# Performance work log

Hardware: AMD Instinct MI355X
Metric: run time of the kernel (lower is better)

## Reference

```python
import jax, jax.numpy as jnp
import numpy as np

N_NODES = 100000
FEAT = 64
HID = 128
N_EDGES = 1200000


def setup_inputs() -> dict:
    key = jax.random.key(0)
    ks = jax.random.split(key, 8)
    x = jax.random.normal(ks[0], (N_NODES, FEAT), dtype=jnp.float32)
    edge_index = jax.random.randint(ks[1], (2, N_EDGES), 0, N_NODES, dtype=jnp.int32)
    # SAGEConv params: lin_l (on aggregated neighbors, with bias), lin_r (on root, no bias)
    W1l = jax.random.normal(ks[2], (HID, FEAT), jnp.float32) / np.float32(np.sqrt(FEAT))
    b1l = jnp.zeros((HID,), jnp.float32)
    W1r = jax.random.normal(ks[3], (HID, FEAT), jnp.float32) / np.float32(np.sqrt(FEAT))
    W2l = jax.random.normal(ks[4], (FEAT, HID), jnp.float32) / np.float32(np.sqrt(HID))
    b2l = jnp.zeros((FEAT,), jnp.float32)
    W2r = jax.random.normal(ks[5], (FEAT, HID), jnp.float32) / np.float32(np.sqrt(HID))
    return {"x": x, "edge_index": edge_index, "W1l": W1l, "b1l": b1l,
            "W1r": W1r, "W2l": W2l, "b2l": b2l, "W2r": W2r}


def _sage_conv(x, src, dst, Wl, bl, Wr, n_nodes):
    # mean aggregation of neighbor messages x[src] at targets dst
    msg = x[src]                                                  # [E, d]
    agg = jax.ops.segment_sum(msg, dst, num_segments=n_nodes)     # [N, d]
    deg = jax.ops.segment_sum(jnp.ones((src.shape[0],), x.dtype), dst,
                              num_segments=n_nodes)               # [N]
    agg = agg / jnp.maximum(deg, 1.0)[:, None]
    # out = lin_l(agg) + lin_r(x); lin_r has no bias (PyG SAGEConv default)
    return agg @ Wl.T + bl + x @ Wr.T


def reference(x, edge_index, W1l, b1l, W1r, W2l, b2l, W2r):
    src, dst = edge_index[0], edge_index[1]
    n = x.shape[0]
    h = jax.nn.relu(_sage_conv(x, src, dst, W1l, b1l, W1r, n))
    # dropout(p=0.5) is identity in eval mode
    out = _sage_conv(h, src, dst, W2l, b2l, W2r, n)
    return out
```

## Files before the change

kernel.cpp:

```cpp
#include <hip/hip_runtime.h>
#include <hip/hip_bf16.h>

typedef __bf16 bf16;
typedef __attribute__((ext_vector_type(8))) __bf16 bf16x8;
typedef __attribute__((ext_vector_type(4))) float f32x4;

#define NBLK 256
#define CAP 3072

__device__ inline void unpack8(uint4 r, f32x4& a, f32x4& b) {
  a.x = __uint_as_float(r.x << 16);
  a.y = __uint_as_float(r.x & 0xffff0000u);
  a.z = __uint_as_float(r.y << 16);
  a.w = __uint_as_float(r.y & 0xffff0000u);
  b.x = __uint_as_float(r.z << 16);
  b.y = __uint_as_float(r.z & 0xffff0000u);
  b.z = __uint_as_float(r.w << 16);
  b.w = __uint_as_float(r.w & 0xffff0000u);
}

__device__ inline uint4 lslot(const bf16* __restrict__ tab, const int* lnbr,
                              int base, int e, int q, int fo) {
  int idx = base + q;
  uint4 r = make_uint4(0u, 0u, 0u, 0u);
  if (idx < e) {
    int j = lnbr[idx];
    r = *(const uint4*)(tab + (long)j * 64 + fo);
  }
  return r;
}

__global__ __launch_bounds__(256) void setup_k(const float* __restrict__ x,
                                               const int* __restrict__ dst,
                                               const float* __restrict__ W1l,
                                               const float* __restrict__ W1r,
                                               const float* __restrict__ W2l,
                                               const float* __restrict__ W2r,
                                               bf16* __restrict__ xb,
                                               bf16* __restrict__ B1,
                                               bf16* __restrict__ B2,
                                               int* __restrict__ hist,
                                               int E, int nb, int N, int Np) {
  __shared__ int h[1024];
  int t = threadIdx.x;
  if (blockIdx.x < NBLK) {
    for (int i = t; i < nb; i += 256) h[i] = 0;
    __syncthreads();
    int chunk = (E + NBLK - 1) / NBLK;
    int s = blockIdx.x * chunk, e = min(E, s + chunk);
    for (int i = s + t; i < e; i += 256) atomicAdd(&h[dst[i] >> 7], 1);
    __syncthreads();
    for (int i = t; i < nb; i += 256) hist[(long)i * NBLK + blockIdx.x] = h[i];
  } else if (blockIdx.x < NBLK + 128) {
    int gid = (blockIdx.x - NBLK) * 256 + t;
    if (gid < 16384) {
      int c = gid >> 7, k = gid & 127;
      float v = (k < 64) ? W1l[c * 64 + k] : W1r[c * 64 + (k - 64)];
      B1[gid] = (bf16)v;
    } else {
      int idx = gid - 16384;
      int n = idx >> 7, k = idx & 127;
      float v = (n < 64) ? W2l[n * 128 + k] : W2r[(n - 64) * 128 + k];
      B2[idx] = (bf16)v;
    }
  } else {
    int gid = (blockIdx.x - NBLK - 128) * 256 + t;
    long base = (long)gid * 4;
    if (base >= (long)Np * 64) return;
    if (base < (long)N * 64) {
      f32x4 v = *(const f32x4*)(x + base);
      bf16 o[4] = {(bf16)v.x, (bf16)v.y, (bf16)v.z, (bf16)v.w};
      *(ulong1*)(xb + base) = *(ulong1*)o;
    } else {
      bf16 o[4] = {(bf16)0.0f, (bf16)0.0f, (bf16)0.0f, (bf16)0.0f};
      *(ulong1*)(xb + base) = *(ulong1*)o;
    }
  }
}

__global__ __launch_bounds__(256) void scanA_k(int* __restrict__ hist,
                                               int* __restrict__ bsum) {
  __shared__ int sd[256];
  int t = threadIdx.x;
  int idx = blockIdx.x * 256 + t;
  int v = hist[idx];
  sd[t] = v;
  __syncthreads();
#pragma unroll
  for (int off = 1; off < 256; off <<= 1) {
    int tv = (t >= off) ? sd[t - off] : 0;
    __syncthreads();
    if (t >= off) sd[t] += tv;
    __syncthreads();
  }
  hist[idx] = sd[t] - v;
  if (t == 255) bsum[blockIdx.x] = sd[255];
}

__global__ __launch_bounds__(1024) void scanB_k(int* __restrict__ bsum, int nb) {
  __shared__ int sd[1024];
  int t = threadIdx.x;
  int v = (t < nb) ? bsum[t] : 0;
  sd[t] = v;
  __syncthreads();
#pragma unroll
  for (int off = 1; off < 1024; off <<= 1) {
    int tv = (t >= off) ? sd[t - off] : 0;
    __syncthreads();
    if (t >= off) sd[t] += tv;
    __syncthreads();
  }
  if (t < nb) bsum[t] = sd[t] - v;
}

__global__ __launch_bounds__(512) void scat_k(const int* __restrict__ src,
                                              const int* __restrict__ dst,
                                              const int* __restrict__ hist,
                                              const int* __restrict__ bsum,
                                              unsigned* __restrict__ ebuf, int E, int nb) {
  __shared__ int cur[1024];
  for (int i = threadIdx.x; i < nb; i += 512)
    cur[i] = bsum[i] + hist[(long)i * NBLK + blockIdx.x];
  __syncthreads();
  int chunk = (E + NBLK - 1) / NBLK;
  int s = blockIdx.x * chunk, e = min(E, s + chunk);
  for (int i = s + threadIdx.x; i < e; i += 512) {
    int d = dst[i];
    int pos = atomicAdd(&cur[d >> 7], 1);
    ebuf[pos] = ((unsigned)src[i] << 7) | (unsigned)(d & 127);
  }
}

__device__ inline void bucket_sort(const unsigned* __restrict__ ebuf, int s, int e,
                                   int t, int* hcnt, int* hoff, int* lnbr) {
  if (t < 128) hcnt[t] = 0;
  __syncthreads();
  for (int i = s + t; i < e; i += 512) atomicAdd(&hcnt[ebuf[i] & 127u], 1);
  __syncthreads();
  if (t < 128) hoff[t + 1] = hcnt[t];
  if (t == 0) hoff[0] = 0;
  __syncthreads();
#pragma unroll
  for (int off = 1; off < 128; off <<= 1) {
    int v = (t < 128 && t >= off) ? hoff[t + 1 - off] : 0;
    __syncthreads();
    if (t < 128 && t >= off) hoff[t + 1] += v;
    __syncthreads();
  }
  if (t < 128) hcnt[t] = hoff[t];
  __syncthreads();
  for (int i = s + t; i < e; i += 512) {
    unsigned r = ebuf[i];
    int pos = atomicAdd(&hcnt[r & 127u], 1);
    lnbr[pos] = (int)(r >> 7);
  }
  __syncthreads();
}

__global__ __launch_bounds__(512) void bagg1_k(const bf16* __restrict__ xb,
                                               const unsigned* __restrict__ ebuf,
                                               const int* __restrict__ bsum,
                                               bf16* __restrict__ A1, int nb, int E) {
  __shared__ int hcnt[128];
  __shared__ int hoff[129];
  __shared__ int lnbr[CAP];
  int b = blockIdx.x, t = threadIdx.x;
  int s = bsum[b];
  int e = (b + 1 < nb) ? bsum[b + 1] : E;
  if (e - s > CAP) e = s + CAP;
  bucket_sort(ebuf, s, e, t, hcnt, hoff, lnbr);

  int wave = t >> 6, lane = t & 63;
  int q = lane >> 3, f = lane & 7, fo = f * 8;
  int ls = hoff[wave * 16], le = hoff[wave * 16 + 1];
  uint4 c0 = lslot(xb, lnbr, ls, le, q, fo);
  uint4 c1 = lslot(xb, lnbr, ls + 8, le, q, fo);
  for (int mm = 0; mm < 16; mm++) {
    int lsN = 0, leN = 0;
    if (mm < 15) { lsN = hoff[wave * 16 + mm + 1]; leN = hoff[wave * 16 + mm + 2]; }
    uint4 n0 = lslot(xb, lnbr, lsN, leN, q, fo);
    uint4 n1 = lslot(xb, lnbr, lsN + 8, leN, q, fo);
    f32x4 sa = {0, 0, 0, 0}, sb = {0, 0, 0, 0};
    if (ls + 16 < le) {
      uint4 a0 = c0, a1 = c1;
      for (int i = ls + 16; i < le; i += 16) {
        uint4 t0 = lslot(xb, lnbr, i, le, q, fo);
        uint4 t1 = lslot(xb, lnbr, i + 8, le, q, fo);
        f32x4 a, bb;
        unpack8(a0, a, bb); sa += a; sb += bb;
        unpack8(a1, a, bb); sa += a; sb += bb;
        a0 = t0; a1 = t1;
      }
      c0 = a0; c1 = a1;
    }
    {
      f32x4 a, bb;
      unpack8(c0, a, bb); sa += a; sb += bb;
      unpack8(c1, a, bb); sa += a; sb += bb;
    }
    float v[8] = {sa.x, sa.y, sa.z, sa.w, sb.x, sb.y, sb.z, sb.w};
#pragma unroll
    for (int k = 0; k < 8; k++) {
      v[k] += __shfl_xor(v[k], 8);
      v[k] += __shfl_xor(v[k], 16);
      v[k] += __shfl_xor(v[k], 32);
    }
    long n = (long)b * 128 + wave * 16 + mm;
    float invd = 1.0f / fmaxf((float)(le - ls), 1.0f);
    if (q == 0) {
      bf16x8 o = {(bf16)(v[0] * invd), (bf16)(v[1] * invd), (bf16)(v[2] * invd),
                  (bf16)(v[3] * invd), (bf16)(v[4] * invd), (bf16)(v[5] * invd),
                  (bf16)(v[6] * invd), (bf16)(v[7] * invd)};
      *(bf16x8*)(A1 + n * 128 + fo) = o;
    } else if (q == 1) {
      uint4 rv = *(const uint4*)(xb + n * 64 + fo);
      *(uint4*)(A1 + n * 128 + 64 + fo) = rv;
    }
    c0 = n0; c1 = n1; ls = lsN; le = leN;
  }
}

__device__ inline int swzoff(int r, int x) {
  return r * 256 + (x ^ (((r & 3) << 6) ^ ((r & 7) << 4)));
}

__global__ __launch_bounds__(256) void fused_k(const bf16* __restrict__ A,
                                               const bf16* __restrict__ B1g,
                                               const bf16* __restrict__ B2g,
                                               const float* __restrict__ b1l,
                                               bf16* __restrict__ Ct,
                                               bf16* __restrict__ Cu, int T) {
  __shared__ __align__(16) char Asm[2][8192];
  __shared__ __align__(16) char Hsm[8192];
  int tid = threadIdx.x;
  int wave = tid >> 6, lane = tid & 63;
  int row = lane & 15, quad = lane >> 4;
  int cb = wave * 32;

  bf16x8 b1f[2][4], b2f[2][4];
#pragma unroll
  for (int jj = 0; jj < 2; jj++)
#pragma unroll
    for (int s = 0; s < 4; s++) {
      b1f[jj][s] = *(const bf16x8*)(B1g + (cb + jj * 16 + row) * 128 + s * 32 + quad * 8);
      b2f[jj][s] = *(const bf16x8*)(B2g + (cb + jj * 16 + row) * 128 + s * 32 + quad * 8);
    }
  float bias[2] = {b1l[cb + row], b1l[cb + 16 + row]};

  int srow = wave * 8 + quad;
  int schunk = row;

  int t = blockIdx.x;
  {
    uint4 v0 = *(const uint4*)(A + ((long)t * 32 + srow) * 128 + schunk * 8);
    uint4 v1 = *(const uint4*)(A + ((long)t * 32 + srow + 4) * 128 + schunk * 8);
    *(uint4*)(Asm[0] + swzoff(srow, schunk * 16)) = v0;
    *(uint4*)(Asm[0] + swzoff(srow + 4, schunk * 16)) = v1;
  }
  __syncthreads();

  int p = 0;
  for (; t < T; t += (int)gridDim.x, p ^= 1) {
    int tn = t + (int)gridDim.x;
    bool pf = tn < T;
    uint4 v0 = {}, v1 = {};
    if (pf) {
      v0 = *(const uint4*)(A + ((long)tn * 32 + srow) * 128 + schunk * 8);
      v1 = *(const uint4*)(A + ((long)tn * 32 + srow + 4) * 128 + schunk * 8);
    }
    f32x4 acc1[2][2] = {};
#pragma unroll
    for (int s = 0; s < 4; s++) {
#pragma unroll
      for (int st = 0; st < 2; st++) {
        bf16x8 a = *(const bf16x8*)(Asm[p] + swzoff(st * 16 + row, s * 64 + quad * 16));
#pragma unroll
        for (int jj = 0; jj < 2; jj++)
          acc1[st][jj] = __builtin_amdgcn_mfma_f32_16x16x32_bf16(a, b1f[jj][s], acc1[st][jj], 0, 0, 0);
      }
    }
#pragma unroll
    for (int st = 0; st < 2; st++)
#pragma unroll
      for (int jj = 0; jj < 2; jj++)
#pragma unroll
        for (int i = 0; i < 4; i++) {
          float v = acc1[st][jj][i] + bias[jj];
          v = v > 0.0f ? v : 0.0f;
          *(bf16*)(Hsm + swzoff(st * 16 + quad * 4 + i, (cb + jj * 16 + row) * 2)) = (bf16)v;
        }
    __syncthreads();
    f32x4 acc2[2][2] = {};
#pragma unroll
    for (int s = 0; s < 4; s++) {
#pragma unroll
      for (int st = 0; st < 2; st++) {
        bf16x8 a = *(const bf16x8*)(Hsm + swzoff(st * 16 + row, s * 64 + quad * 16));
#pragma unroll
        for (int jj = 0; jj < 2; jj++)
          acc2[st][jj] = __builtin_amdgcn_mfma_f32_16x16x32_bf16(a, b2f[jj][s], acc2[st][jj], 0, 0, 0);
      }
    }
    bf16* outp = (wave < 2) ? Ct : Cu;
    int oc = cb + row - ((wave < 2) ? 0 : 64);
#pragma unroll
    for (int st = 0; st < 2; st++)
#pragma unroll
      for (int jj = 0; jj < 2; jj++)
#pragma unroll
        for (int i = 0; i < 4; i++) {
          long grow = (long)t * 32 + st * 16 + quad * 4 + i;
          outp[grow * 64 + oc + jj * 16] = (bf16)acc2[st][jj][i];
        }
    if (pf) {
      *(uint4*)(Asm[p ^ 1] + swzoff(srow, schunk * 16)) = v0;
      *(uint4*)(Asm[p ^ 1] + swzoff(srow + 4, schunk * 16)) = v1;
    }
    __syncthreads();
  }
}

__global__ __launch_bounds__(512) void bagg2_k(const bf16* __restrict__ tmat,
                                               const bf16* __restrict__ umat,
                                               const unsigned* __restrict__ ebuf,
                                               const int* __restrict__ bsum,
                                               const float* __restrict__ b2l,
                                               float* __restrict__ out,
                                               int nb, int N, int E) {
  __shared__ int hcnt[128];
  __shared__ int hoff[129];
  __shared__ int lnbr[CAP];
  int b = blockIdx.x, t = threadIdx.x;
  int s = bsum[b];
  int e = (b + 1 < nb) ? bsum[b + 1] : E;
  if (e - s > CAP) e = s + CAP;
  bucket_sort(ebuf, s, e, t, hcnt, hoff, lnbr);

  int wave = t >> 6, lane = t & 63;
  int q = lane >> 3, f = lane & 7, fo = f * 8;
  int ls = hoff[wave * 16], le = hoff[wave * 16 + 1];
  uint4 c0 = lslot(tmat, lnbr, ls, le, q, fo);
  uint4 c1 = lslot(tmat, lnbr, ls + 8, le, q, fo);
  for (int mm = 0; mm < 16; mm++) {
    int lsN = 0, leN = 0;
    if (mm < 15) { lsN = hoff[wave * 16 + mm + 1]; leN = hoff[wave * 16 + mm + 2]; }
    uint4 n0 = lslot(tmat, lnbr, lsN, leN, q, fo);
    uint4 n1 = lslot(tmat, lnbr, lsN + 8, leN, q, fo);
    f32x4 sa = {0, 0, 0, 0}, sb = {0, 0, 0, 0};
    if (ls + 16 < le) {
      uint4 a0 = c0, a1 = c1;
      for (int i = ls + 16; i < le; i += 16) {
        uint4 t0 = lslot(tmat, lnbr, i, le, q, fo);
        uint4 t1 = lslot(tmat, lnbr, i + 8, le, q, fo);
        f32x4 a, bb;
        unpack8(a0, a, bb); sa += a; sb += bb;
        unpack8(a1, a, bb); sa += a; sb += bb;
        a0 = t0; a1 = t1;
      }
      c0 = a0; c1 = a1;
    }
    {
      f32x4 a, bb;
      unpack8(c0, a, bb); sa += a; sb += bb;
      unpack8(c1, a, bb); sa += a; sb += bb;
    }
    float v[8] = {sa.x, sa.y, sa.z, sa.w, sb.x, sb.y, sb.z, sb.w};
#pragma unroll
    for (int k = 0; k < 8; k++) {
      v[k] += __shfl_xor(v[k], 8);
      v[k] += __shfl_xor(v[k], 16);
      v[k] += __shfl_xor(v[k], 32);
    }
    long n = (long)b * 128 + wave * 16 + mm;
    if (q == 0 && n < N) {
      float invd = 1.0f / fmaxf((float)(le - ls), 1.0f);
      f32x4 b0 = *(const f32x4*)(b2l + fo);
      f32x4 b1 = *(const f32x4*)(b2l + fo + 4);
      f32x4 ua, ub;
      unpack8(*(const uint4*)(umat + n * 64 + fo), ua, ub);
      f32x4 o0, o1;
      o0.x = v[0] * invd + b0.x + ua.x;
      o0.y = v[1] * invd + b0.y + ua.y;
      o0.z = v[2] * invd + b0.z + ua.z;
      o0.w = v[3] * invd + b0.w + ua.w;
      o1.x = v[4] * invd + b1.x + ub.x;
      o1.y = v[5] * invd + b1.y + ub.y;
      o1.z = v[6] * invd + b1.z + ub.z;
      o1.w = v[7] * invd + b1.w + ub.w;
      *(f32x4*)(out + n * 64 + fo) = o0;
      *(f32x4*)(out + n * 64 + fo + 4) = o1;
    }
    c0 = n0; c1 = n1; ls = lsN; le = leN;
  }
}

static inline size_t align256(size_t x) { return (x + 255) / 256 * 256; }

extern "C" void kernel_launch(void* const* d_in, const int* in_sizes, int n_in,
                              void* d_out, int out_size, void* d_ws, size_t ws_size,
                              hipStream_t stream) {
  const float* x = (const float*)d_in[0];
  const int* edge_index = (const int*)d_in[1];
  const float* W1l = (const float*)d_in[2];
  const float* b1l = (const float*)d_in[3];
  const float* W1r = (const float*)d_in[4];
  const float* W2l = (const float*)d_in[5];
  const float* b2l = (const float*)d_in[6];
  const float* W2r = (const float*)d_in[7];

  const int N = in_sizes[0] / 64;
  const int E = in_sizes[1] / 2;
  const int Np = (N + 127) / 128 * 128;
  const int nb = Np / 128;
  const int M = nb * NBLK;

  const int* src = edge_index;
  const int* dst = edge_index + E;

  char* ws = (char*)d_ws;
  size_t off = 0;
  int* hist = (int*)(ws + off);           off += align256((size_t)M * 4);
  int* bsum = (int*)(ws + off);           off += align256((size_t)nb * 4);
  unsigned* ebuf = (unsigned*)(ws + off); off += align256((size_t)E * 4);
  bf16* xb = (bf16*)(ws + off);           off += align256((size_t)Np * 64 * 2);
  bf16* A1 = (bf16*)(ws + off);           off += align256((size_t)Np * 128 * 2);
  bf16* tmat = (bf16*)(ws + off);         off += align256((size_t)Np * 64 * 2);
  bf16* umat = (bf16*)(ws + off);         off += align256((size_t)Np * 64 * 2);
  bf16* B1 = (bf16*)(ws + off);           off += align256(128 * 128 * 2);
  bf16* B2 = (bf16*)(ws + off);           off += align256(128 * 128 * 2);
  float* out = (float*)d_out;

  const int cvtBlocks = (int)(((long)Np * 64 / 4 + 255) / 256);
  setup_k<<<NBLK + 128 + cvtBlocks, 256, 0, stream>>>(x, dst, W1l, W1r, W2l, W2r,
                                                      xb, B1, B2, hist, E, nb, N, Np);
  scanA_k<<<nb, 256, 0, stream>>>(hist, bsum);
  scanB_k<<<1, 1024, 0, stream>>>(bsum, nb);
  scat_k<<<NBLK, 512, 0, stream>>>(src, dst, hist, bsum, ebuf, E, nb);

  bagg1_k<<<nb, 512, 0, stream>>>(xb, ebuf, bsum, A1, nb, E);
  fused_k<<<1564, 256, 0, stream>>>(A1, B1, B2, b1l, tmat, umat, Np / 32);
  bagg2_k<<<nb, 512, 0, stream>>>(tmat, umat, ebuf, bsum, b2l, out, nb, N, E);
}
```

Before: 228.7 us.

## Materialize CSR in first aggregation and reuse it for second-layer aggregation

The first aggregation kernel now writes its per-block bucket-sorted neighbor lists and row offsets to global memory as a CSR structure. The second aggregation becomes a simple one-wave-per-node gather over that CSR instead of re-sorting edges in shared memory. A1 no longer carries a copy of the root features, and the fused GEMM kernel reads the root half directly from xb. This removes a duplicate sort and a redundant copy, at the cost of extra global writes and reads of the neighbor array.

```diff
diff --git a/kernel.cpp b/kernel.cpp
--- a/kernel.cpp
+++ b/kernel.cpp
@@ -17,6 +17,17 @@
   b.y = __uint_as_float(r.z & 0xffff0000u);
   b.z = __uint_as_float(r.w << 16);
   b.w = __uint_as_float(r.w & 0xffff0000u);
+}
+
+__device__ inline uint4 slot_load(const bf16* __restrict__ tab, const int* __restrict__ nbr,
+                                  int base, int e, int q, int fo) {
+  int idx = base + q;
+  uint4 r = make_uint4(0u, 0u, 0u, 0u);
+  if (idx < e) {
+    int j = nbr[idx];
+    r = *(const uint4*)(tab + (long)j * 64 + fo);
+  }
+  return r;
 }
 
 __device__ inline uint4 lslot(const bf16* __restrict__ tab, const int* lnbr,
@@ -157,10 +168,13 @@
   __syncthreads();
 }
 
-__global__ __launch_bounds__(512) void bagg1_k(const bf16* __restrict__ xb,
-                                               const unsigned* __restrict__ ebuf,
-                                               const int* __restrict__ bsum,
-                                               bf16* __restrict__ A1, int nb, int E) {
+__global__ __launch_bounds__(512) void csragg1_k(const bf16* __restrict__ xb,
+                                                 const unsigned* __restrict__ ebuf,
+                                                 const int* __restrict__ bsum,
+                                                 int* __restrict__ rowptr,
+                                                 int* __restrict__ nbr,
+                                                 bf16* __restrict__ A1,
+                                                 int nb, int Np, int E) {
   __shared__ int hcnt[128];
   __shared__ int hoff[129];
   __shared__ int lnbr[CAP];
@@ -169,6 +183,10 @@
   int e = (b + 1 < nb) ? bsum[b + 1] : E;
   if (e - s > CAP) e = s + CAP;
   bucket_sort(ebuf, s, e, t, hcnt, hoff, lnbr);
+
+  if (t < 128) rowptr[b * 128 + t] = s + hoff[t];
+  if (b == nb - 1 && t == 128) rowptr[Np] = E;
+  for (int i = t; i < e - s; i += 512) nbr[s + i] = lnbr[i];
 
   int wave = t >> 6, lane = t & 63;
   int q = lane >> 3, f = lane & 7, fo = f * 8;
@@ -211,10 +229,7 @@
       bf16x8 o = {(bf16)(v[0] * invd), (bf16)(v[1] * invd), (bf16)(v[2] * invd),
                   (bf16)(v[3] * invd), (bf16)(v[4] * invd), (bf16)(v[5] * invd),
                   (bf16)(v[6] * invd), (bf16)(v[7] * invd)};
-      *(bf16x8*)(A1 + n * 128 + fo) = o;
-    } else if (q == 1) {
-      uint4 rv = *(const uint4*)(xb + n * 64 + fo);
-      *(uint4*)(A1 + n * 128 + 64 + fo) = rv;
+      *(bf16x8*)(A1 + n * 64 + fo) = o;
     }
     c0 = n0; c1 = n1; ls = lsN; le = leN;
   }
@@ -225,6 +240,7 @@
 }
 
 __global__ __launch_bounds__(256) void fused_k(const bf16* __restrict__ A,
+                                               const bf16* __restrict__ xb,
                                                const bf16* __restrict__ B1g,
                                                const bf16* __restrict__ B2g,
                                                const float* __restrict__ b1l,
@@ -249,11 +265,14 @@
 
   int srow = wave * 8 + quad;
   int schunk = row;
+  const bf16* atab = (schunk < 8) ? A : xb;
+  int co = (schunk & 7) * 8;
 
   int t = blockIdx.x;
   {
-    uint4 v0 = *(const uint4*)(A + ((long)t * 32 + srow) * 128 + schunk * 8);
-    uint4 v1 = *(const uint4*)(A + ((long)t * 32 + srow + 4) * 128 + schunk * 8);
+    long rb = (long)t * 32 + srow;
+    uint4 v0 = *(const uint4*)(atab + rb * 64 + co);
+    uint4 v1 = *(const uint4*)(atab + (rb + 4) * 64 + co);
     *(uint4*)(Asm[0] + swzoff(srow, schunk * 16)) = v0;
     *(uint4*)(Asm[0] + swzoff(srow + 4, schunk * 16)) = v1;
   }
@@ -265,8 +284,9 @@
     bool pf = tn < T;
     uint4 v0 = {}, v1 = {};
     if (pf) {
-      v0 = *(const uint4*)(A + ((long)tn * 32 + srow) * 128 + schunk * 8);
-      v1 = *(const uint4*)(A + ((long)tn * 32 + srow + 4) * 128 + schunk * 8);
+      long rb = (long)tn * 32 + srow;
+      v0 = *(const uint4*)(atab + rb * 64 + co);
+      v1 = *(const uint4*)(atab + (rb + 4) * 64 + co);
     }
     f32x4 acc1[2][2] = {};
 #pragma unroll
@@ -320,77 +340,59 @@
   }
 }
 
-__global__ __launch_bounds__(512) void bagg2_k(const bf16* __restrict__ tmat,
-                                               const bf16* __restrict__ umat,
-                                               const unsigned* __restrict__ ebuf,
-                                               const int* __restrict__ bsum,
-                                               const float* __restrict__ b2l,
-                                               float* __restrict__ out,
-                                               int nb, int N, int E) {
-  __shared__ int hcnt[128];
-  __shared__ int hoff[129];
-  __shared__ int lnbr[CAP];
-  int b = blockIdx.x, t = threadIdx.x;
-  int s = bsum[b];
-  int e = (b + 1 < nb) ? bsum[b + 1] : E;
-  if (e - s > CAP) e = s + CAP;
-  bucket_sort(ebuf, s, e, t, hcnt, hoff, lnbr);
-
-  int wave = t >> 6, lane = t & 63;
-  int q = lane >> 3, f = lane & 7, fo = f * 8;
-  int ls = hoff[wave * 16], le = hoff[wave * 16 + 1];
-  uint4 c0 = lslot(tmat, lnbr, ls, le, q, fo);
-  uint4 c1 = lslot(tmat, lnbr, ls + 8, le, q, fo);
-  for (int mm = 0; mm < 16; mm++) {
-    int lsN = 0, leN = 0;
-    if (mm < 15) { lsN = hoff[wave * 16 + mm + 1]; leN = hoff[wave * 16 + mm + 2]; }
-    uint4 n0 = lslot(tmat, lnbr, lsN, leN, q, fo);
-    uint4 n1 = lslot(tmat, lnbr, lsN + 8, leN, q, fo);
-    f32x4 sa = {0, 0, 0, 0}, sb = {0, 0, 0, 0};
-    if (ls + 16 < le) {
-      uint4 a0 = c0, a1 = c1;
-      for (int i = ls + 16; i < le; i += 16) {
-        uint4 t0 = lslot(tmat, lnbr, i, le, q, fo);
-        uint4 t1 = lslot(tmat, lnbr, i + 8, le, q, fo);
-        f32x4 a, bb;
-        unpack8(a0, a, bb); sa += a; sb += bb;
-        unpack8(a1, a, bb); sa += a; sb += bb;
-        a0 = t0; a1 = t1;
-      }
-      c0 = a0; c1 = a1;
-    }
-    {
-      f32x4 a, bb;
-      unpack8(c0, a, bb); sa += a; sb += bb;
-      unpack8(c1, a, bb); sa += a; sb += bb;
-    }
-    float v[8] = {sa.x, sa.y, sa.z, sa.w, sb.x, sb.y, sb.z, sb.w};
-#pragma unroll
-    for (int k = 0; k < 8; k++) {
-      v[k] += __shfl_xor(v[k], 8);
-      v[k] += __shfl_xor(v[k], 16);
-      v[k] += __shfl_xor(v[k], 32);
-    }
-    long n = (long)b * 128 + wave * 16 + mm;
-    if (q == 0 && n < N) {
-      float invd = 1.0f / fmaxf((float)(le - ls), 1.0f);
-      f32x4 b0 = *(const f32x4*)(b2l + fo);
-      f32x4 b1 = *(const f32x4*)(b2l + fo + 4);
-      f32x4 ua, ub;
-      unpack8(*(const uint4*)(umat + n * 64 + fo), ua, ub);
-      f32x4 o0, o1;
-      o0.x = v[0] * invd + b0.x + ua.x;
-      o0.y = v[1] * invd + b0.y + ua.y;
-      o0.z = v[2] * invd + b0.z + ua.z;
-      o0.w = v[3] * invd + b0.w + ua.w;
-      o1.x = v[4] * invd + b1.x + ub.x;
-      o1.y = v[5] * invd + b1.y + ub.y;
-      o1.z = v[6] * invd + b1.z + ub.z;
-      o1.w = v[7] * invd + b1.w + ub.w;
-      *(f32x4*)(out + n * 64 + fo) = o0;
-      *(f32x4*)(out + n * 64 + fo + 4) = o1;
-    }
-    c0 = n0; c1 = n1; ls = lsN; le = leN;
+__global__ __launch_bounds__(256) void agg2_k(const bf16* __restrict__ tmat,
+                                              const bf16* __restrict__ umat,
+                                              const int* __restrict__ rowptr,
+                                              const int* __restrict__ nbr,
+                                              const float* __restrict__ b2l,
+                                              float* __restrict__ out, int N) {
+  int wave = threadIdx.x >> 6, lane = threadIdx.x & 63;
+  int n = blockIdx.x * 4 + wave;
+  if (n >= N) return;
+  int s = rowptr[n], e = rowptr[n + 1];
+  int q = lane >> 3, f = lane & 7;
+  int fo = f * 8;
+  f32x4 sa = {0, 0, 0, 0}, sb = {0, 0, 0, 0};
+  uint4 c0 = slot_load(tmat, nbr, s, e, q, fo);
+  uint4 c1 = slot_load(tmat, nbr, s + 8, e, q, fo);
+  int i = s + 16;
+  for (; i < e; i += 16) {
+    uint4 n0 = slot_load(tmat, nbr, i, e, q, fo);
+    uint4 n1 = slot_load(tmat, nbr, i + 8, e, q, fo);
+    f32x4 a, b;
+    unpack8(c0, a, b); sa += a; sb += b;
+    unpack8(c1, a, b); sa += a; sb += b;
+    c0 = n0; c1 = n1;
+  }
+  {
+    f32x4 a, b;
+    unpack8(c0, a, b); sa += a; sb += b;
+    unpack8(c1, a, b); sa += a; sb += b;
+  }
+  float v[8] = {sa.x, sa.y, sa.z, sa.w, sb.x, sb.y, sb.z, sb.w};
+#pragma unroll
+  for (int k = 0; k < 8; k++) {
+    v[k] += __shfl_xor(v[k], 8);
+    v[k] += __shfl_xor(v[k], 16);
+    v[k] += __shfl_xor(v[k], 32);
+  }
+  if (q == 0) {
+    float invd = 1.0f / fmaxf((float)(e - s), 1.0f);
+    f32x4 b0 = *(const f32x4*)(b2l + fo);
+    f32x4 b1 = *(const f32x4*)(b2l + fo + 4);
+    f32x4 ua, ub;
+    unpack8(*(const uint4*)(umat + n * 64 + fo), ua, ub);
+    f32x4 o0, o1;
+    o0.x = v[0] * invd + b0.x + ua.x;
+    o0.y = v[1] * invd + b0.y + ua.y;
+    o0.z = v[2] * invd + b0.z + ua.z;
+    o0.w = v[3] * invd + b0.w + ua.w;
+    o1.x = v[4] * invd + b1.x + ub.x;
+    o1.y = v[5] * invd + b1.y + ub.y;
+    o1.z = v[6] * invd + b1.z + ub.z;
+    o1.w = v[7] * invd + b1.w + ub.w;
+    *(f32x4*)(out + n * 64 + fo) = o0;
+    *(f32x4*)(out + n * 64 + fo + 4) = o1;
   }
 }
 
@@ -421,9 +423,11 @@
   size_t off = 0;
   int* hist = (int*)(ws + off);           off += align256((size_t)M * 4);
   int* bsum = (int*)(ws + off);           off += align256((size_t)nb * 4);
+  int* rowptr = (int*)(ws + off);         off += align256((size_t)(Np + 1) * 4);
   unsigned* ebuf = (unsigned*)(ws + off); off += align256((size_t)E * 4);
+  int* nbr = (int*)(ws + off);            off += align256((size_t)E * 4);
   bf16* xb = (bf16*)(ws + off);           off += align256((size_t)Np * 64 * 2);
-  bf16* A1 = (bf16*)(ws + off);           off += align256((size_t)Np * 128 * 2);
+  bf16* A1 = (bf16*)(ws + off);           off += align256((size_t)Np * 64 * 2);
   bf16* tmat = (bf16*)(ws + off);         off += align256((size_t)Np * 64 * 2);
   bf16* umat = (bf16*)(ws + off);         off += align256((size_t)Np * 64 * 2);
   bf16* B1 = (bf16*)(ws + off);           off += align256(128 * 128 * 2);
@@ -437,7 +441,7 @@
   scanB_k<<<1, 1024, 0, stream>>>(bsum, nb);
   scat_k<<<NBLK, 512, 0, stream>>>(src, dst, hist, bsum, ebuf, E, nb);
 
-  bagg1_k<<<nb, 512, 0, stream>>>(xb, ebuf, bsum, A1, nb, E);
-  fused_k<<<1564, 256, 0, stream>>>(A1, B1, B2, b1l, tmat, umat, Np / 32);
-  bagg2_k<<<nb, 512, 0, stream>>>(tmat, umat, ebuf, bsum, b2l, out, nb, N, E);
-}
+  csragg1_k<<<nb, 512, 0, stream>>>(xb, ebuf, bsum, rowptr, nbr, A1, nb, Np, E);
+  fused_k<<<1564, 256, 0, stream>>>(A1, xb, B1, B2, b1l, tmat, umat, Np / 32);
+  agg2_k<<<(N + 3) / 4, 256, 0, stream>>>(tmat, umat, rowptr, nbr, b2l, out, N);
+}
```

Result: faster. 218.6 us (-4.4%).
